# Kernel optimization log

Measured on AMD Instinct MI355X. Metric: run time of the kernel, lower is better.

Reference implementation:

```python
import jax, jax.numpy as jnp
import numpy as np

BATCH, SEQ, DMODEL, DHID = 4, 4096, 1024, 1024
R_MIN, R_MAX = 0.9, 0.99
MAX_PHASE = np.pi / 50  # module overrides ctor arg with pi/50
EPS = 1e-5


def setup_inputs() -> dict:
    key = jax.random.key(0)
    ks = jax.random.split(key, 8)
    # nu_init
    u1 = jax.random.uniform(ks[0], (DHID,)) * (1 - EPS) + EPS
    mag_sq = u1 * (R_MAX ** 2 - R_MIN ** 2) + R_MIN ** 2
    nu_log = jnp.log(-0.5 * jnp.log(mag_sq + EPS))
    # theta_init
    u2 = jax.random.uniform(ks[1], (DHID,)) * (1 - EPS) + EPS
    theta_log = jnp.log(MAX_PHASE * u2)
    B_re = jax.random.normal(ks[2], (DHID, DMODEL)) / np.sqrt(2 * DMODEL)
    B_im = jax.random.normal(ks[3], (DHID, DMODEL)) / np.sqrt(2 * DMODEL)
    C_re = jax.random.normal(ks[4], (DMODEL, DHID)) / np.sqrt(DHID)
    C_im = jax.random.normal(ks[5], (DMODEL, DHID)) / np.sqrt(DHID)
    D_skip = jax.random.normal(ks[6], (DMODEL,))
    inputs = jax.random.normal(ks[7], (BATCH, SEQ, DMODEL), dtype=jnp.float32)
    return {"inputs": inputs, "nu_log": nu_log, "theta_log": theta_log,
            "B_re": B_re, "B_im": B_im, "C_re": C_re, "C_im": C_im,
            "D_skip": D_skip}


def reference(inputs, nu_log, theta_log, B_re, B_im, C_re, C_im, D_skip):
    nu = jnp.exp(nu_log)
    theta = jnp.exp(theta_log)
    diag_lambda = jnp.exp(-nu + 1j * theta)            # [H] complex
    # forward recomputes gamma_log from nu_log (parameter gamma_log unused)
    gamma_log = 0.5 * jnp.log(1 - jnp.exp(-2 * jnp.exp(nu_log)) + EPS)
    B_norm = (B_re + 1j * B_im) * jnp.exp(gamma_log)[:, None]  # [H, D]
    inputs_c = inputs.astype(jnp.complex64)
    Bu = jnp.einsum('hd,btd->bth', B_norm, inputs_c)   # [B, T, H]

    def step(h, bu_t):
        h = diag_lambda * h + bu_t
        return h, h

    h0 = jnp.zeros((inputs.shape[0], diag_lambda.shape[0]), dtype=Bu.dtype)
    _, hs = jax.lax.scan(step, h0, jnp.swapaxes(Bu, 0, 1))  # [T, B, H]
    hs = jnp.swapaxes(hs, 0, 1)                              # [B, T, H]
    C_complex = C_re + 1j * C_im                              # [D, H]
    out = jnp.einsum('bth,dh->btd', hs, C_complex).real + inputs * D_skip
    return out.astype(jnp.float32)
```

## Files before the change

### kernel.cpp

```cpp
#include <hip/hip_runtime.h>


typedef __bf16 bf16x8 __attribute__((ext_vector_type(8)));
typedef float floatx4 __attribute__((ext_vector_type(4)));

__device__ __forceinline__ unsigned short f2bf(float f) {
  unsigned u = __float_as_uint(f);
  u += 0x7fffu + ((u >> 16) & 1u);
  return (unsigned short)(u >> 16);
}
__device__ __forceinline__ float bf2f(unsigned short s) {
  return __uint_as_float(((unsigned)s) << 16);
}


__global__ void prep_params(const float* __restrict__ nu_log,
                            const float* __restrict__ theta_log,
                            float* __restrict__ lam,
                            float* __restrict__ lamL,
                            float* __restrict__ gamma)
{
  int h = blockIdx.x * 256 + threadIdx.x;
  float nu = expf(nu_log[h]);
  float th = expf(theta_log[h]);
  float r = expf(-nu);
  lam[h]        = r * cosf(th);
  lam[1024 + h] = r * sinf(th);
  float rL = expf(-128.0f * nu);
  lamL[h]        = rL * cosf(128.0f * th);
  lamL[1024 + h] = rL * sinf(128.0f * th);
  gamma[h] = sqrtf(1.0f - expf(-2.0f * nu) + 1e-5f);
}

__global__ void prep_B(const float* __restrict__ B_re, const float* __restrict__ B_im,
                       const float* __restrict__ gamma, unsigned short* __restrict__ Bcat)
{
  int tid = blockIdx.x * 256 + threadIdx.x;
  int n = tid >> 10;
  int d = tid & 1023;
  int h = n & 1023;
  float v = (n < 1024 ? B_re[h * 1024 + d] : B_im[h * 1024 + d]) * gamma[h];
  Bcat[tid] = f2bf(v);
}

__global__ void prep_C(const float* __restrict__ C_re, const float* __restrict__ C_im,
                       unsigned short* __restrict__ Ccat)
{
  int tid = blockIdx.x * 256 + threadIdx.x;
  int d = tid >> 11;
  int k = tid & 2047;
  float v = (k < 1024) ? C_re[d * 1024 + k] : -C_im[d * 1024 + (k - 1024)];
  Ccat[tid] = f2bf(v);
}

__global__ void conv_inputs(const float* __restrict__ in, unsigned short* __restrict__ outb)
{
  int tid = blockIdx.x * 256 + threadIdx.x;
  float4 v = ((const float4*)in)[tid];
  unsigned lo = (unsigned)f2bf(v.x) | ((unsigned)f2bf(v.y) << 16);
  unsigned hi = (unsigned)f2bf(v.z) | ((unsigned)f2bf(v.w) << 16);
  ((uint2*)outb)[tid] = make_uint2(lo, hi);
}


template <int EPI>
__global__ __launch_bounds__(256) void gemm_bt_kernel(
    const unsigned short* __restrict__ A,
    const unsigned short* __restrict__ Bt,
    void* __restrict__ Cout,
    int M, int N, int K,
    const float* __restrict__ skip_in,
    const float* __restrict__ skip_w)
{
  __shared__ unsigned short As[2][128 * 32];
  __shared__ unsigned short Bs[2][128 * 32];

  const int tid  = threadIdx.x;
  const int lane = tid & 63;
  const int wave = tid >> 6;
  const int wm = wave >> 1;
  const int wn = wave & 1;

  const int flat    = blockIdx.x;
  const int xcd     = flat & 7;
  const int local   = flat >> 3;
  const int m_tile  = xcd * 16 + (local & 15);
  const int n_tile  = local >> 4;
  const int m0 = m_tile * 128;
  const int n0 = n_tile * 128;

  const int ldr = lane >> 2;
  const int pos = lane & 3;
  const int lm  = lane & 15;
  const int q   = lane >> 4;

  const int r0 = wave * 32 + ldr;
  const int ca0 = pos ^ ((r0 >> 1) & 3);
  const int r1 = r0 + 16;
  const int ca1 = pos ^ ((r1 >> 1) & 3);

  const unsigned short* gA0 = A  + (size_t)(m0 + r0) * K + ca0 * 8;
  const unsigned short* gA1 = A  + (size_t)(m0 + r1) * K + ca1 * 8;
  const unsigned short* gB0 = Bt + (size_t)(n0 + r0) * K + ca0 * 8;
  const unsigned short* gB1 = Bt + (size_t)(n0 + r1) * K + ca1 * 8;
  const int lofs0 = r0 * 32 + pos * 8;
  const int lofs1 = r1 * 32 + pos * 8;

  floatx4 acc[4][4];
#pragma unroll
  for (int i = 0; i < 4; ++i)
#pragma unroll
    for (int j = 0; j < 4; ++j)
      acc[i][j] = (floatx4){0.f, 0.f, 0.f, 0.f};

  {
    __builtin_amdgcn_global_load_lds(
        (const __attribute__((address_space(1))) void*)gA0,
        (__attribute__((address_space(3))) void*)&As[0][lofs0], 16, 0, 0);
    __builtin_amdgcn_global_load_lds(
        (const __attribute__((address_space(1))) void*)gA1,
        (__attribute__((address_space(3))) void*)&As[0][lofs1], 16, 0, 0);
    __builtin_amdgcn_global_load_lds(
        (const __attribute__((address_space(1))) void*)gB0,
        (__attribute__((address_space(3))) void*)&Bs[0][lofs0], 16, 0, 0);
    __builtin_amdgcn_global_load_lds(
        (const __attribute__((address_space(1))) void*)gB1,
        (__attribute__((address_space(3))) void*)&Bs[0][lofs1], 16, 0, 0);
  }

  int cur = 0;
  for (int kt = 0; kt < K; kt += 32) {
    __syncthreads();

    const int nxt = cur ^ 1;
    if (kt + 32 < K) {
      const int ko = kt + 32;
      __builtin_amdgcn_global_load_lds(
          (const __attribute__((address_space(1))) void*)(gA0 + ko),
          (__attribute__((address_space(3))) void*)&As[nxt][lofs0], 16, 0, 0);
      __builtin_amdgcn_global_load_lds(
          (const __attribute__((address_space(1))) void*)(gA1 + ko),
          (__attribute__((address_space(3))) void*)&As[nxt][lofs1], 16, 0, 0);
      __builtin_amdgcn_global_load_lds(
          (const __attribute__((address_space(1))) void*)(gB0 + ko),
          (__attribute__((address_space(3))) void*)&Bs[nxt][lofs0], 16, 0, 0);
      __builtin_amdgcn_global_load_lds(
          (const __attribute__((address_space(1))) void*)(gB1 + ko),
          (__attribute__((address_space(3))) void*)&Bs[nxt][lofs1], 16, 0, 0);
    }

    bf16x8 afrag[4], bfrag[4];
#pragma unroll
    for (int i = 0; i < 4; ++i) {
      const int r = wm * 64 + i * 16 + lm;
      afrag[i] = *reinterpret_cast<const bf16x8*>(&As[cur][r * 32 + (q ^ ((r >> 1) & 3)) * 8]);
    }
#pragma unroll
    for (int j = 0; j < 4; ++j) {
      const int r = wn * 64 + j * 16 + lm;
      bfrag[j] = *reinterpret_cast<const bf16x8*>(&Bs[cur][r * 32 + (q ^ ((r >> 1) & 3)) * 8]);
    }
#pragma unroll
    for (int i = 0; i < 4; ++i)
#pragma unroll
      for (int j = 0; j < 4; ++j)
        acc[i][j] = __builtin_amdgcn_mfma_f32_16x16x32_bf16(afrag[i], bfrag[j], acc[i][j], 0, 0, 0);

    cur = nxt;
  }

#pragma unroll
  for (int i = 0; i < 4; ++i) {
#pragma unroll
    for (int j = 0; j < 4; ++j) {
      const int row0 = m0 + wm * 64 + i * 16 + q * 4;
      const int col  = n0 + wn * 64 + j * 16 + lm;
#pragma unroll
      for (int r = 0; r < 4; ++r) {
        const size_t idx = (size_t)(row0 + r) * N + col;
        if (EPI == 0) {
          ((unsigned short*)Cout)[idx] = f2bf(acc[i][j][r]);
        } else {
          ((float*)Cout)[idx] = acc[i][j][r] + skip_in[idx] * skip_w[col];
        }
      }
    }
  }
}


__global__ void scan_finals(const unsigned short* __restrict__ Bu,
                            const float* __restrict__ lam,
                            float2* __restrict__ finals)
{
  int tid = blockIdx.x * 256 + threadIdx.x;
  int h = tid & 1023, c = (tid >> 10) & 31, b = tid >> 15;
  float lre = lam[h], lim = lam[1024 + h];
  const unsigned short* p = Bu + ((size_t)(b * 4096 + c * 128) * 2048) + h;
  float yre = 0.f, yim = 0.f;
#pragma unroll 4
  for (int t = 0; t < 128; ++t) {
    float ure = bf2f(p[0]);
    float uim = bf2f(p[1024]);
    float nre = fmaf(lre, yre, fmaf(-lim, yim, ure));
    float nim = fmaf(lre, yim, fmaf(lim, yre, uim));
    yre = nre; yim = nim;
    p += 2048;
  }
  finals[tid] = make_float2(yre, yim);
}

__global__ void scan_carries(const float2* __restrict__ finals,
                             const float* __restrict__ lamL,
                             float2* __restrict__ carry)
{
  int tid = blockIdx.x * 256 + threadIdx.x;
  int h = tid & 1023, b = tid >> 10;
  float Lre = lamL[h], Lim = lamL[1024 + h];
  float Hre = 0.f, Him = 0.f;
  for (int c = 0; c < 32; ++c) {
    size_t i = ((size_t)(b * 32 + c) << 10) + h;
    carry[i] = make_float2(Hre, Him);
    float2 f = finals[i];
    float nre = fmaf(Lre, Hre, fmaf(-Lim, Him, f.x));
    float nim = fmaf(Lre, Him, fmaf(Lim, Hre, f.y));
    Hre = nre; Him = nim;
  }
}

__global__ void scan_apply(const float* __restrict__ lam,
                           const float2* __restrict__ carry,
                           unsigned short* __restrict__ Bu)
{
  int tid = blockIdx.x * 256 + threadIdx.x;
  int h = tid & 1023, c = (tid >> 10) & 31, b = tid >> 15;
  float lre = lam[h], lim = lam[1024 + h];
  float2 cv = carry[tid];
  float yre = cv.x, yim = cv.y;
  unsigned short* p = Bu + ((size_t)(b * 4096 + c * 128) * 2048) + h;
#pragma unroll 4
  for (int t = 0; t < 128; ++t) {
    float ure = bf2f(p[0]);
    float uim = bf2f(p[1024]);
    float nre = fmaf(lre, yre, fmaf(-lim, yim, ure));
    float nim = fmaf(lre, yim, fmaf(lim, yre, uim));
    yre = nre; yim = nim;
    p[0]    = f2bf(yre);
    p[1024] = f2bf(yim);
    p += 2048;
  }
}


extern "C" void kernel_launch(void* const* d_in, const int* in_sizes, int n_in,
                              void* d_out, int out_size, void* d_ws, size_t ws_size,
                              hipStream_t stream)
{
  const float* inputs    = (const float*)d_in[0];
  const float* nu_log    = (const float*)d_in[1];
  const float* theta_log = (const float*)d_in[2];
  const float* B_re      = (const float*)d_in[3];
  const float* B_im      = (const float*)d_in[4];
  const float* C_re      = (const float*)d_in[5];
  const float* C_im      = (const float*)d_in[6];
  const float* D_skip    = (const float*)d_in[7];
  float* out = (float*)d_out;

  char* ws = (char*)d_ws;
  float* lam   = (float*)ws;
  float* lamL  = lam + 2048;
  float* gamma = lamL + 2048;
  unsigned short* inp_bf = (unsigned short*)(ws + (1 << 16));
  unsigned short* Bcat   = inp_bf + (size_t)16384 * 1024;
  unsigned short* Ccat   = Bcat   + (size_t)2048 * 1024;
  unsigned short* Bu     = Ccat   + (size_t)1024 * 2048;
  float2* finals = (float2*)(Bu + (size_t)16384 * 2048);
  float2* carry  = finals + 131072;

  prep_params<<<4,    256, 0, stream>>>(nu_log, theta_log, lam, lamL, gamma);
  prep_B     <<<8192, 256, 0, stream>>>(B_re, B_im, gamma, Bcat);
  prep_C     <<<8192, 256, 0, stream>>>(C_re, C_im, Ccat);
  conv_inputs<<<16384,256, 0, stream>>>(inputs, inp_bf);

  gemm_bt_kernel<0><<<2048, 256, 0, stream>>>(
      inp_bf, Bcat, Bu, 16384, 2048, 1024, nullptr, nullptr);

  scan_finals <<<512, 256, 0, stream>>>(Bu, lam, finals);
  scan_carries<<<16,  256, 0, stream>>>(finals, lamL, carry);
  scan_apply  <<<512, 256, 0, stream>>>(lam, carry, Bu);

  gemm_bt_kernel<1><<<1024, 256, 0, stream>>>(
      Bu, Ccat, out, 16384, 1024, 2048, inputs, D_skip);
}
```

Baseline: 363.6 us.

## Use 256x256 GEMM tiles with 512 threads and a 4-stage LDS ring

Both GEMMs move from 128x128 tiles with 256 threads and double buffering to 256x256 tiles with 8 waves. Each wave now computes a 128x64 sub-tile. Global-to-LDS loads run three stages ahead in a 4-buffer ring, with explicit vmcnt waits and barriers, and MFMA sections are wrapped in s_setprio. The aim is higher data reuse per loaded byte and better hiding of load latency. In exchange it uses about 128KB of LDS and more accumulator registers per thread, which limits the CU to one block and gives fewer blocks per launch (512 and 256).

After: 363.0 us. Within noise of the previous version (-0.1%).

```diff
diff --git a/kernel.cpp b/kernel.cpp
--- a/kernel.cpp
+++ b/kernel.cpp
@@ -63,8 +63,51 @@
 }
 
 
+#define GLDS(gp, lp) __builtin_amdgcn_global_load_lds(                        \
+      (const __attribute__((address_space(1))) void*)(gp),                    \
+      (__attribute__((address_space(3))) void*)(lp), 16, 0, 0)
+
+#define STAGE(kt, buf) do {                                                   \
+    const int _ko = (kt) * 32;                                                \
+    GLDS(gA0 + _ko, &As[(buf)][lofs0]);                                       \
+    GLDS(gA1 + _ko, &As[(buf)][lofs1]);                                       \
+    GLDS(gB0 + _ko, &Bs[(buf)][lofs0]);                                       \
+    GLDS(gB1 + _ko, &Bs[(buf)][lofs1]);                                       \
+  } while (0)
+
+#define BODY(buf) do {                                                        \
+    bf16x8 af[8], bf[4];                                                      \
+    _Pragma("unroll")                                                         \
+    for (int i = 0; i < 8; ++i) {                                             \
+      const int r = wm * 128 + i * 16 + lm;                                   \
+      af[i] = *reinterpret_cast<const bf16x8*>(                               \
+          &As[(buf)][r * 32 + (q ^ ((r >> 1) & 3)) * 8]);                     \
+    }                                                                         \
+    _Pragma("unroll")                                                         \
+    for (int j = 0; j < 4; ++j) {                                             \
+      const int r = wn * 64 + j * 16 + lm;                                    \
+      bf[j] = *reinterpret_cast<const bf16x8*>(                               \
+          &Bs[(buf)][r * 32 + (q ^ ((r >> 1) & 3)) * 8]);                     \
+    }                                                                         \
+    __builtin_amdgcn_s_setprio(1);                                            \
+    _Pragma("unroll")                                                         \
+    for (int i = 0; i < 8; ++i)                                               \
+      _Pragma("unroll")                                                       \
+      for (int j = 0; j < 4; ++j)                                             \
+        acc[i][j] = __builtin_amdgcn_mfma_f32_16x16x32_bf16(                  \
+            af[i], bf[j], acc[i][j], 0, 0, 0);                                \
+    __builtin_amdgcn_s_setprio(0);                                            \
+  } while (0)
+
+#define RING_SYNC(vm) do {                                                    \
+    __builtin_amdgcn_sched_barrier(0);                                        \
+    asm volatile("s_waitcnt vmcnt(" #vm ")" ::: "memory");                    \
+    __builtin_amdgcn_s_barrier();                                             \
+    asm volatile("" ::: "memory");                                            \
+  } while (0)
+
 template <int EPI>
-__global__ __launch_bounds__(256) void gemm_bt_kernel(
+__global__ __launch_bounds__(512, 2) void gemm256_kernel(
     const unsigned short* __restrict__ A,
     const unsigned short* __restrict__ Bt,
     void* __restrict__ Cout,
@@ -72,22 +115,22 @@
     const float* __restrict__ skip_in,
     const float* __restrict__ skip_w)
 {
-  __shared__ unsigned short As[2][128 * 32];
-  __shared__ unsigned short Bs[2][128 * 32];
+  __shared__ __align__(16) unsigned short As[4][256 * 32];
+  __shared__ __align__(16) unsigned short Bs[4][256 * 32];
 
   const int tid  = threadIdx.x;
   const int lane = tid & 63;
   const int wave = tid >> 6;
-  const int wm = wave >> 1;
-  const int wn = wave & 1;
+  const int wm = wave >> 2;
+  const int wn = wave & 3;
 
   const int flat    = blockIdx.x;
   const int xcd     = flat & 7;
   const int local   = flat >> 3;
-  const int m_tile  = xcd * 16 + (local & 15);
-  const int n_tile  = local >> 4;
-  const int m0 = m_tile * 128;
-  const int n0 = n_tile * 128;
+  const int m_tile  = xcd * 8 + (local & 7);
+  const int n_tile  = local >> 3;
+  const int m0 = m_tile * 256;
+  const int n0 = n_tile * 256;
 
   const int ldr = lane >> 2;
   const int pos = lane & 3;
@@ -95,8 +138,8 @@
   const int q   = lane >> 4;
 
   const int r0 = wave * 32 + ldr;
+  const int r1 = r0 + 16;
   const int ca0 = pos ^ ((r0 >> 1) & 3);
-  const int r1 = r0 + 16;
   const int ca1 = pos ^ ((r1 >> 1) & 3);
 
   const unsigned short* gA0 = A  + (size_t)(m0 + r0) * K + ca0 * 8;
@@ -106,74 +149,38 @@
   const int lofs0 = r0 * 32 + pos * 8;
   const int lofs1 = r1 * 32 + pos * 8;
 
-  floatx4 acc[4][4];
-#pragma unroll
-  for (int i = 0; i < 4; ++i)
+  floatx4 acc[8][4];
+#pragma unroll
+  for (int i = 0; i < 8; ++i)
 #pragma unroll
     for (int j = 0; j < 4; ++j)
       acc[i][j] = (floatx4){0.f, 0.f, 0.f, 0.f};
 
-  {
-    __builtin_amdgcn_global_load_lds(
-        (const __attribute__((address_space(1))) void*)gA0,
-        (__attribute__((address_space(3))) void*)&As[0][lofs0], 16, 0, 0);
-    __builtin_amdgcn_global_load_lds(
-        (const __attribute__((address_space(1))) void*)gA1,
-        (__attribute__((address_space(3))) void*)&As[0][lofs1], 16, 0, 0);
-    __builtin_amdgcn_global_load_lds(
-        (const __attribute__((address_space(1))) void*)gB0,
-        (__attribute__((address_space(3))) void*)&Bs[0][lofs0], 16, 0, 0);
-    __builtin_amdgcn_global_load_lds(
-        (const __attribute__((address_space(1))) void*)gB1,
-        (__attribute__((address_space(3))) void*)&Bs[0][lofs1], 16, 0, 0);
-  }
-
-  int cur = 0;
-  for (int kt = 0; kt < K; kt += 32) {
-    __syncthreads();
-
-    const int nxt = cur ^ 1;
-    if (kt + 32 < K) {
-      const int ko = kt + 32;
-      __builtin_amdgcn_global_load_lds(
-          (const __attribute__((address_space(1))) void*)(gA0 + ko),
-          (__attribute__((address_space(3))) void*)&As[nxt][lofs0], 16, 0, 0);
-      __builtin_amdgcn_global_load_lds(
-          (const __attribute__((address_space(1))) void*)(gA1 + ko),
-          (__attribute__((address_space(3))) void*)&As[nxt][lofs1], 16, 0, 0);
-      __builtin_amdgcn_global_load_lds(
-          (const __attribute__((address_space(1))) void*)(gB0 + ko),
-          (__attribute__((address_space(3))) void*)&Bs[nxt][lofs0], 16, 0, 0);
-      __builtin_amdgcn_global_load_lds(
-          (const __attribute__((address_space(1))) void*)(gB1 + ko),
-          (__attribute__((address_space(3))) void*)&Bs[nxt][lofs1], 16, 0, 0);
-    }
-
-    bf16x8 afrag[4], bfrag[4];
-#pragma unroll
-    for (int i = 0; i < 4; ++i) {
-      const int r = wm * 64 + i * 16 + lm;
-      afrag[i] = *reinterpret_cast<const bf16x8*>(&As[cur][r * 32 + (q ^ ((r >> 1) & 3)) * 8]);
-    }
+  const int KT = K >> 5;
+
+  STAGE(0, 0);
+  STAGE(1, 1);
+  STAGE(2, 2);
+  asm volatile("s_waitcnt vmcnt(8)" ::: "memory");
+  __builtin_amdgcn_s_barrier();
+  asm volatile("" ::: "memory");
+
+  for (int kt = 0; kt + 3 < KT; ++kt) {
+    STAGE(kt + 3, (kt + 3) & 3);
+    BODY(kt & 3);
+    RING_SYNC(8);
+  }
+  BODY((KT - 3) & 3);
+  RING_SYNC(4);
+  BODY((KT - 2) & 3);
+  RING_SYNC(0);
+  BODY((KT - 1) & 3);
+
+#pragma unroll
+  for (int i = 0; i < 8; ++i) {
 #pragma unroll
     for (int j = 0; j < 4; ++j) {
-      const int r = wn * 64 + j * 16 + lm;
-      bfrag[j] = *reinterpret_cast<const bf16x8*>(&Bs[cur][r * 32 + (q ^ ((r >> 1) & 3)) * 8]);
-    }
-#pragma unroll
-    for (int i = 0; i < 4; ++i)
-#pragma unroll
-      for (int j = 0; j < 4; ++j)
-        acc[i][j] = __builtin_amdgcn_mfma_f32_16x16x32_bf16(afrag[i], bfrag[j], acc[i][j], 0, 0, 0);
-
-    cur = nxt;
-  }
-
-#pragma unroll
-  for (int i = 0; i < 4; ++i) {
-#pragma unroll
-    for (int j = 0; j < 4; ++j) {
-      const int row0 = m0 + wm * 64 + i * 16 + q * 4;
+      const int row0 = m0 + wm * 128 + i * 16 + q * 4;
       const int col  = n0 + wn * 64 + j * 16 + lm;
 #pragma unroll
       for (int r = 0; r < 4; ++r) {
@@ -282,13 +289,13 @@
   prep_C     <<<8192, 256, 0, stream>>>(C_re, C_im, Ccat);
   conv_inputs<<<16384,256, 0, stream>>>(inputs, inp_bf);
 
-  gemm_bt_kernel<0><<<2048, 256, 0, stream>>>(
+  gemm256_kernel<0><<<512, 512, 0, stream>>>(
       inp_bf, Bcat, Bu, 16384, 2048, 1024, nullptr, nullptr);
 
   scan_finals <<<512, 256, 0, stream>>>(Bu, lam, finals);
   scan_carries<<<16,  256, 0, stream>>>(finals, lamL, carry);
   scan_apply  <<<512, 256, 0, stream>>>(lam, carry, Bu);
 
-  gemm_bt_kernel<1><<<1024, 256, 0, stream>>>(
+  gemm256_kernel<1><<<256, 512, 0, stream>>>(
       Bu, Ccat, out, 16384, 1024, 2048, inputs, D_skip);
 }
```
